# Kernel optimization log

Measured on AMD Instinct MI355X. Metric: run time of the kernel, lower is better.

Reference implementation:

```python
import jax, jax.numpy as jnp
import numpy as np

N_CLASSES = 91

def setup_inputs() -> dict:
    key = jax.random.key(0)
    k1, k2 = jax.random.split(key)
    B, H, W = 32, 1024, 1024
    inputs = jax.random.randint(k1, (B, H, W), 0, N_CLASSES, dtype=jnp.int32)
    targets = jax.random.randint(k2, (B, H, W), 0, N_CLASSES, dtype=jnp.int32)
    smooth = jnp.ones((1,), dtype=jnp.float32)  # original default smooth=1
    return {"inputs": inputs, "targets": targets, "smooth": smooth}

def reference(inputs, targets, smooth):
    # Single-pass histogram formulation of the original 91-iteration loop.
    B = inputs.shape[0]
    x = inputs.reshape(B, -1)   # [B, N] int labels
    t = targets.reshape(B, -1)  # [B, N]
    rows = jnp.arange(B)[:, None]
    # per-class counts: cnt_x[b,c] = #pixels with x==c (== a.sum per class)
    cnt_x = jnp.zeros((B, N_CLASSES), jnp.float32).at[rows, x].add(1.0)
    cnt_t = jnp.zeros((B, N_CLASSES), jnp.float32).at[rows, t].add(1.0)
    # intersection[b,c] = #pixels with x==t==c; route mismatches to a dump bin
    match = jnp.where(x == t, x, N_CLASSES)
    inter = jnp.zeros((B, N_CLASSES + 1), jnp.float32).at[rows, match].add(1.0)[:, :N_CLASSES]
    union = cnt_x + cnt_t - inter  # total - intersection
    s = smooth[0]
    iou = (inter + s) / (union + s)  # [B, C]
    return iou.mean(axis=1)          # sum_IoU / n_classes, shape [B]
```

## Files before the change

### kernel.cpp

```cpp
#include <hip/hip_runtime.h>

#define NC 91
#define NB 32
#define HW (1024 * 1024)

#define THREADS 256
#define PPT 64
#define PIX_PER_BLOCK (THREADS * PPT)
#define WPT 23


__device__ __forceinline__ void proc_pixel(int x, int t, int* hp, int* s_inter) {
    const int wx = x >> 2, wt = t >> 2;
    const int ix = 1 << ((x & 3) << 3);
    const int it = 1 << ((t & 3) << 3);
    const int vx = hp[wx];
    const int vt = hp[wt];
    hp[wt] = vt + it;
    hp[wx] = vx + ix + (wx == wt ? it : 0);
    if (x == t) atomicAdd(&s_inter[x], 1);
}

__global__ __launch_bounds__(256) void hist_kernel(const int* __restrict__ x,
                                                   const int* __restrict__ t,
                                                   int* __restrict__ g_hist,
                                                   int* __restrict__ g_inter) {
    __shared__ int s_hist[THREADS * WPT];
    __shared__ int s_inter[NC];
    __shared__ int s_p[8][WPT * 4];

    const int tid = threadIdx.x;
    int* hp = &s_hist[tid * WPT];
#pragma unroll
    for (int j = 0; j < WPT; ++j) hp[j] = 0;
    if (tid < NC) s_inter[tid] = 0;
    __syncthreads();

    const int b = blockIdx.y;
    const long base = (long)b * HW + (long)blockIdx.x * PIX_PER_BLOCK;
    const int4* __restrict__ x4 = (const int4*)(x + base);
    const int4* __restrict__ t4 = (const int4*)(t + base);

#pragma unroll 4
    for (int i = 0; i < PPT / 4; ++i) {
        int4 xv = x4[i * THREADS + tid];
        int4 tv = t4[i * THREADS + tid];
        proc_pixel(xv.x, tv.x, hp, s_inter);
        proc_pixel(xv.y, tv.y, hp, s_inter);
        proc_pixel(xv.z, tv.z, hp, s_inter);
        proc_pixel(xv.w, tv.w, hp, s_inter);
    }
    __syncthreads();

    const int chunk = tid >> 5;
    const int w = tid & 31;
    if (w < WPT) {
        int f0 = 0, f1 = 0, f2 = 0, f3 = 0;
        const int kb = chunk * 32;
        for (int k = 0; k < 32; ++k) {
            unsigned v = (unsigned)s_hist[(kb + k) * WPT + w];
            f0 += (int)(v & 0xffu);
            f1 += (int)((v >> 8) & 0xffu);
            f2 += (int)((v >> 16) & 0xffu);
            f3 += (int)(v >> 24);
        }
        s_p[chunk][w * 4 + 0] = f0;
        s_p[chunk][w * 4 + 1] = f1;
        s_p[chunk][w * 4 + 2] = f2;
        s_p[chunk][w * 4 + 3] = f3;
    }
    __syncthreads();

    if (tid < NC) {
        int sum = 0;
#pragma unroll
        for (int ch = 0; ch < 8; ++ch) sum += s_p[ch][tid];
        if (sum) atomicAdd(&g_hist[b * NC + tid], sum);
        const int in = s_inter[tid];
        if (in)  atomicAdd(&g_inter[b * NC + tid], in);
    }
}

__global__ __launch_bounds__(64) void finalize_kernel(const int* __restrict__ g_hist,
                                                      const int* __restrict__ g_inter,
                                                      const float* __restrict__ smooth,
                                                      float* __restrict__ out) {
    const int b = blockIdx.x;
    const int lane = threadIdx.x;
    const float s = smooth[0];
    float acc = 0.0f;
    for (int c = lane; c < NC; c += 64) {
        float in = (float)g_inter[b * NC + c];
        float ht = (float)g_hist[b * NC + c];
        acc += (in + s) / (ht - in + s);
    }
#pragma unroll
    for (int off = 32; off > 0; off >>= 1)
        acc += __shfl_down(acc, off, 64);
    if (lane == 0) out[b] = acc / (float)NC;
}

extern "C" void kernel_launch(void* const* d_in, const int* in_sizes, int n_in,
                              void* d_out, int out_size, void* d_ws, size_t ws_size,
                              hipStream_t stream) {
    const int* x = (const int*)d_in[0];
    const int* t = (const int*)d_in[1];
    const float* smooth = (const float*)d_in[2];
    float* out = (float*)d_out;

    int* g_hist = (int*)d_ws;
    int* g_inter = g_hist + NB * NC;

    hipMemsetAsync(d_ws, 0, 2 * NB * NC * sizeof(int), stream);

    dim3 grid(HW / PIX_PER_BLOCK, NB);
    hist_kernel<<<grid, THREADS, 0, stream>>>(x, t, g_hist, g_inter);
    finalize_kernel<<<NB, 64, 0, stream>>>(g_hist, g_inter, smooth, out);
}
```

Measured before the change: 286.9 us.

## Replace per-thread packed histograms with 8 shared atomic copies and prefetch

```diff
diff --git a/kernel.cpp b/kernel.cpp
--- a/kernel.cpp
+++ b/kernel.cpp
@@ -7,74 +7,57 @@
 #define THREADS 256
 #define PPT 64
 #define PIX_PER_BLOCK (THREADS * PPT)
-#define WPT 23
+#define NCOPY 8
 
 
 __device__ __forceinline__ void proc_pixel(int x, int t, int* hp, int* s_inter) {
-    const int wx = x >> 2, wt = t >> 2;
-    const int ix = 1 << ((x & 3) << 3);
-    const int it = 1 << ((t & 3) << 3);
-    const int vx = hp[wx];
-    const int vt = hp[wt];
-    hp[wt] = vt + it;
-    hp[wx] = vx + ix + (wx == wt ? it : 0);
-    if (x == t) atomicAdd(&s_inter[x], 1);
+    atomicAdd(&hp[x], x == t ? 2 : 1);
+    if (x != t) atomicAdd(&hp[t], 1);
+    else        atomicAdd(&s_inter[x], 1);
 }
 
-__global__ __launch_bounds__(256) void hist_kernel(const int* __restrict__ x,
-                                                   const int* __restrict__ t,
-                                                   int* __restrict__ g_hist,
-                                                   int* __restrict__ g_inter) {
-    __shared__ int s_hist[THREADS * WPT];
+__global__ __launch_bounds__(256, 8) void hist_kernel(const int* __restrict__ x,
+                                                      const int* __restrict__ t,
+                                                      int* __restrict__ g_hist,
+                                                      int* __restrict__ g_inter) {
+    __shared__ int s_h[NCOPY * NC];
     __shared__ int s_inter[NC];
-    __shared__ int s_p[8][WPT * 4];
 
     const int tid = threadIdx.x;
-    int* hp = &s_hist[tid * WPT];
-#pragma unroll
-    for (int j = 0; j < WPT; ++j) hp[j] = 0;
+    for (int j = tid; j < NCOPY * NC; j += THREADS) s_h[j] = 0;
     if (tid < NC) s_inter[tid] = 0;
     __syncthreads();
+
+    int* hp = &s_h[(tid & 7) * NC];
 
     const int b = blockIdx.y;
     const long base = (long)b * HW + (long)blockIdx.x * PIX_PER_BLOCK;
     const int4* __restrict__ x4 = (const int4*)(x + base);
     const int4* __restrict__ t4 = (const int4*)(t + base);
 
-#pragma unroll 4
-    for (int i = 0; i < PPT / 4; ++i) {
-        int4 xv = x4[i * THREADS + tid];
-        int4 tv = t4[i * THREADS + tid];
-        proc_pixel(xv.x, tv.x, hp, s_inter);
-        proc_pixel(xv.y, tv.y, hp, s_inter);
-        proc_pixel(xv.z, tv.z, hp, s_inter);
-        proc_pixel(xv.w, tv.w, hp, s_inter);
-    }
-    __syncthreads();
+    const int n = PPT / 4;
+    int4 xv0 = x4[tid],           tv0 = t4[tid];
+    int4 xv1 = x4[THREADS + tid], tv1 = t4[THREADS + tid];
 
-    const int chunk = tid >> 5;
-    const int w = tid & 31;
-    if (w < WPT) {
-        int f0 = 0, f1 = 0, f2 = 0, f3 = 0;
-        const int kb = chunk * 32;
-        for (int k = 0; k < 32; ++k) {
-            unsigned v = (unsigned)s_hist[(kb + k) * WPT + w];
-            f0 += (int)(v & 0xffu);
-            f1 += (int)((v >> 8) & 0xffu);
-            f2 += (int)((v >> 16) & 0xffu);
-            f3 += (int)(v >> 24);
-        }
-        s_p[chunk][w * 4 + 0] = f0;
-        s_p[chunk][w * 4 + 1] = f1;
-        s_p[chunk][w * 4 + 2] = f2;
-        s_p[chunk][w * 4 + 3] = f3;
+    for (int i = 0; i < n; ++i) {
+        const int pf = (i + 2 < n) ? (i + 2) : (n - 1);
+        int4 xn = x4[pf * THREADS + tid];
+        int4 tn = t4[pf * THREADS + tid];
+
+        proc_pixel(xv0.x, tv0.x, hp, s_inter);
+        proc_pixel(xv0.y, tv0.y, hp, s_inter);
+        proc_pixel(xv0.z, tv0.z, hp, s_inter);
+        proc_pixel(xv0.w, tv0.w, hp, s_inter);
+
+        xv0 = xv1; tv0 = tv1;
+        xv1 = xn;  tv1 = tn;
     }
     __syncthreads();
 
     if (tid < NC) {
         int sum = 0;
 #pragma unroll
-        for (int ch = 0; ch < 8; ++ch) sum += s_p[ch][tid];
+        for (int k = 0; k < NCOPY; ++k) sum += s_h[k * NC + tid];
         if (sum) atomicAdd(&g_hist[b * NC + tid], sum);
         const int in = s_inter[tid];
         if (in)  atomicAdd(&g_inter[b * NC + tid], in);
```

New measurement: 281.9 us. Within noise of the previous version (-1.7%).

## Batch four LDS histogram updates and software-pipeline global loads two iterations ahead

Applied to the files above, without the earlier changes.

```diff
diff --git a/kernel.cpp b/kernel.cpp
--- a/kernel.cpp
+++ b/kernel.cpp
@@ -10,21 +10,30 @@
 #define WPT 23
 
 
-__device__ __forceinline__ void proc_pixel(int x, int t, int* hp, int* s_inter) {
-    const int wx = x >> 2, wt = t >> 2;
-    const int ix = 1 << ((x & 3) << 3);
-    const int it = 1 << ((t & 3) << 3);
-    const int vx = hp[wx];
-    const int vt = hp[wt];
-    hp[wt] = vt + it;
-    hp[wx] = vx + ix + (wx == wt ? it : 0);
-    if (x == t) atomicAdd(&s_inter[x], 1);
+__device__ __forceinline__ void batch4(int l0, int l1, int l2, int l3, int* hp) {
+    const int w0 = l0 >> 2, w1 = l1 >> 2, w2 = l2 >> 2, w3 = l3 >> 2;
+    const int o0 = 1 << ((l0 & 3) << 3);
+    const int o1 = 1 << ((l1 & 3) << 3);
+    const int o2 = 1 << ((l2 & 3) << 3);
+    const int o3 = 1 << ((l3 & 3) << 3);
+    const int v0 = hp[w0];
+    const int v1 = hp[w1];
+    const int v2 = hp[w2];
+    const int v3 = hp[w3];
+    const int i1 = o1 + ((w0 == w1) ? o0 : 0);
+    const int i2 = o2 + ((w0 == w2) ? o0 : 0) + ((w1 == w2) ? o1 : 0);
+    const int i3 = o3 + ((w0 == w3) ? o0 : 0) + ((w1 == w3) ? o1 : 0)
+                      + ((w2 == w3) ? o2 : 0);
+    hp[w0] = v0 + o0;
+    hp[w1] = v1 + i1;
+    hp[w2] = v2 + i2;
+    hp[w3] = v3 + i3;
 }
 
-__global__ __launch_bounds__(256) void hist_kernel(const int* __restrict__ x,
-                                                   const int* __restrict__ t,
-                                                   int* __restrict__ g_hist,
-                                                   int* __restrict__ g_inter) {
+__global__ __launch_bounds__(256, 6) void hist_kernel(const int* __restrict__ x,
+                                                      const int* __restrict__ t,
+                                                      int* __restrict__ g_hist,
+                                                      int* __restrict__ g_inter) {
     __shared__ int s_hist[THREADS * WPT];
     __shared__ int s_inter[NC];
     __shared__ int s_p[8][WPT * 4];
@@ -41,14 +50,25 @@
     const int4* __restrict__ x4 = (const int4*)(x + base);
     const int4* __restrict__ t4 = (const int4*)(t + base);
 
-#pragma unroll 4
-    for (int i = 0; i < PPT / 4; ++i) {
-        int4 xv = x4[i * THREADS + tid];
-        int4 tv = t4[i * THREADS + tid];
-        proc_pixel(xv.x, tv.x, hp, s_inter);
-        proc_pixel(xv.y, tv.y, hp, s_inter);
-        proc_pixel(xv.z, tv.z, hp, s_inter);
-        proc_pixel(xv.w, tv.w, hp, s_inter);
+    const int n = PPT / 4;
+    int4 xv0 = x4[tid],           tv0 = t4[tid];
+    int4 xv1 = x4[THREADS + tid], tv1 = t4[THREADS + tid];
+
+    for (int i = 0; i < n; ++i) {
+        const int pf = (i + 2 < n) ? (i + 2) : (n - 1);
+        int4 xn = x4[pf * THREADS + tid];
+        int4 tn = t4[pf * THREADS + tid];
+
+        batch4(xv0.x, tv0.x, xv0.y, tv0.y, hp);
+        batch4(xv0.z, tv0.z, xv0.w, tv0.w, hp);
+
+        if (xv0.x == tv0.x) atomicAdd(&s_inter[xv0.x], 1);
+        if (xv0.y == tv0.y) atomicAdd(&s_inter[xv0.y], 1);
+        if (xv0.z == tv0.z) atomicAdd(&s_inter[xv0.z], 1);
+        if (xv0.w == tv0.w) atomicAdd(&s_inter[xv0.w], 1);
+
+        xv0 = xv1; tv0 = tv1;
+        xv1 = xn;  tv1 = tn;
     }
     __syncthreads();
 
```

Result: no change. 285.7 us (-0.4%).
